# Optimization experiments

Measured on AMD Instinct MI355X. Metric: run time of the kernel, lower is better.

The kernel has to match this reference:

```python
import jax, jax.numpy as jnp
import numpy as np
from jax import lax

NUM_ANCHORS = 3
NUM_CLASSES = 80
SCORE_THRESH = 0.3
NMS_THRESH = 0.45
TOPK = 128  # max kept candidates per class per image (fixed-shape NMS)
REDUCTIONS = (8, 16, 32)
_ANCHORS = np.array([[12, 16], [19, 36], [40, 28], [36, 75], [76, 55], [72, 146],
                     [142, 110], [192, 243], [459, 401]], dtype=np.float32).reshape(3, 3, 2)


def _decode(pred, anchors):
    # pred: [b, A*(5+C), h, w]; anchors: [A,2] already divided by reduction
    b, c, h, w = pred.shape
    p = pred.reshape(b, NUM_ANCHORS, 5 + NUM_CLASSES, h * w).transpose(0, 1, 3, 2)  # [b,A,hw,5+C]
    gx = (jnp.arange(h * w) % w).astype(p.dtype)   # grid x offset per flattened cell
    gy = (jnp.arange(h * w) // w).astype(p.dtype)  # grid y offset
    cx = (jax.nn.sigmoid(p[..., 0]) + gx) / w
    cy = (jax.nn.sigmoid(p[..., 1]) + gy) / h
    bw = jnp.exp(p[..., 2]) * (anchors[:, 0] / w)[None, :, None]
    bh = jnp.exp(p[..., 3]) * (anchors[:, 1] / h)[None, :, None]
    x1 = cx - 0.5 * bw
    y1 = cy - 0.5 * bh
    boxes = jnp.stack([x1, y1, x1 + bw, y1 + bh], axis=-1)  # [b,A,hw,4] xyxy, normalized
    scores = jax.nn.sigmoid(p[..., 4])[..., None] * jax.nn.sigmoid(p[..., 5:])  # [b,A,hw,C]
    return boxes, scores


def _nms_single(boxes, probs):
    # boxes: [N,4]; probs: [N] with below-threshold entries masked to -1.
    # Greedy NMS on top-K candidates sorted by score (same math as the numpy loop).
    vals, idx = lax.top_k(probs, TOPK)
    bx = boxes[idx]                                            # [K,4] sorted by score desc
    area = (bx[:, 2] - bx[:, 0]) * (bx[:, 3] - bx[:, 1])
    tl = jnp.maximum(bx[:, None, :2], bx[None, :, :2])
    br = jnp.minimum(bx[:, None, 2:], bx[None, :, 2:])
    whi = jnp.clip(br - tl, 0.0)
    inter = whi[..., 0] * whi[..., 1]
    iou = inter / (area[:, None] + area[None, :] - inter)      # [K,K]
    ar = jnp.arange(TOPK)

    def step(p, i):
        sup = (iou[i] > NMS_THRESH) & (ar > i) & (p[i] > 0)
        return jnp.where(sup, -1.0, p), None

    p, _ = lax.scan(step, vals, ar)
    keep = p > 0
    return jnp.where(keep[:, None], bx, 0.0), jnp.where(keep, p, 0.0)


def reference(preds0, preds1, preds2):
    boxes_list, score_list = [], []
    for pred, red, anc in zip((preds0, preds1, preds2), REDUCTIONS, _ANCHORS):
        bx, sc = _decode(pred, jnp.asarray(anc) / red)
        boxes_list.append(bx)
        score_list.append(sc)
    boxes = jnp.concatenate(boxes_list, axis=2)
    scores = jnp.concatenate(score_list, axis=2)
    b = boxes.shape[0]
    boxes = boxes.reshape(b, -1, 4)              # [b, N, 4],  N = A * sum(hw)
    scores = scores.reshape(b, -1, NUM_CLASSES)  # [b, N, C]
    probs = jnp.where(scores > SCORE_THRESH, scores, -1.0)
    per_class = jax.vmap(_nms_single, in_axes=(None, 1))        # map over classes
    out_boxes, out_scores = jax.vmap(per_class)(boxes, probs)   # [b,C,K,4], [b,C,K]
    cls_id = jnp.broadcast_to(
        jnp.arange(NUM_CLASSES, dtype=out_boxes.dtype)[None, :, None], out_scores.shape)
    # [b, C, K, 6] = (x1, y1, x2, y2, score, class_id); zeroed rows = no detection
    return jnp.concatenate([out_boxes, out_scores[..., None], cls_id[..., None]], axis=-1)


def setup_inputs():
    key = jax.random.key(0)
    k0, k1, k2 = jax.random.split(key, 3)
    C = NUM_ANCHORS * (5 + NUM_CLASSES)
    return {
        "preds0": jax.random.normal(k0, (16, C, 76, 76), jnp.float32),
        "preds1": jax.random.normal(k1, (16, C, 38, 38), jnp.float32),
        "preds2": jax.random.normal(k2, (16, C, 19, 19), jnp.float32),
    }
```

## Files before the change

kernel.cpp:

```cpp
#include <hip/hip_runtime.h>
#include <math.h>
#include <stdint.h>

#define BATCH 16
#define NCLS 80
#define SUMHW 7581
#define NN 22743
#define ASTRIDE 7584
#define PADNN (3 * ASTRIDE)
#define TOPK 128
#define CAP 1024
#define WCAP 320
#define GMAX (4 * WCAP)
#define PRUNECAP 512
#define KEYBASE 0x3E800000u
#define KB2     0x3F180000u
#define SBITS   0x3F19999Au

typedef float f32x4 __attribute__((ext_vector_type(4)));

__device__ __forceinline__ float sigf(float x) {
    float e = (float)exp(-(double)x);
    return 1.0f / (1.0f + e);
}
__device__ __forceinline__ float expf_cr(float x) {
    return (float)exp((double)x);
}

struct DecParams { float aw[9]; float ah[9]; };

__global__ __launch_bounds__(256) void decode_kernel(
        const float* __restrict__ p0, const float* __restrict__ p1,
        const float* __restrict__ p2,
        float* __restrict__ so_arr, float* __restrict__ xthr_arr) {
    int blk = blockIdx.x;
    int b = blk / 27;
    int rem = blk % 27;
    int a = rem / 9;
    int seg = rem % 9;
    int s, segi;
    if (seg < 6)      { s = 0; segi = seg; }
    else if (seg < 8) { s = 1; segi = seg - 6; }
    else              { s = 2; segi = 0; }
    const int HW_[3]  = {5776, 1444, 361};
    const int OFF_[3] = {0, 5776, 7220};
    const float* __restrict__ pr = (s == 0) ? p0 : (s == 1) ? p1 : p2;
    int HW = HW_[s], OFF = OFF_[s];
    int t = threadIdx.x;

    auto mkthr = [](float so) {
        float thr = __int_as_float(0x7F800000);
        if (so > 0.59999f) {
            double arg = (double)so / 0.59999 - 1.0;
            thr = __double2float_rd(-log(arg));
        }
        return thr;
    };

    if (s != 2) {
        int cell0 = segi * 1024 + t * 4;
        if (cell0 >= HW) return;
        const float4* ob4 =
            (const float4*)(pr + ((size_t)b * 255 + (size_t)a * 85 + 4) * (size_t)HW);
        float4 ov = ob4[cell0 >> 2];
        float4 sov, thv;
        sov.x = sigf(ov.x); thv.x = mkthr(sov.x);
        sov.y = sigf(ov.y); thv.y = mkthr(sov.y);
        sov.z = sigf(ov.z); thv.z = mkthr(sov.z);
        sov.w = sigf(ov.w); thv.w = mkthr(sov.w);
        size_t pidx = (size_t)b * PADNN + a * ASTRIDE + OFF + cell0;
        *(float4*)(so_arr + pidx)   = sov;
        *(float4*)(xthr_arr + pidx) = thv;
    } else {
        const float* ob = pr + ((size_t)b * 255 + (size_t)a * 85 + 4) * 361;
        for (int i = t; i < 361; i += 256) {
            float so = sigf(ob[i]);
            size_t pidx = (size_t)b * PADNN + a * ASTRIDE + 7220 + i;
            so_arr[pidx] = so;
            xthr_arr[pidx] = mkthr(so);
        }
    }
}

__global__ __launch_bounds__(256) void select_nms_kernel(
        const float* __restrict__ p0, const float* __restrict__ p1,
        const float* __restrict__ p2,
        const float* __restrict__ so_arr,
        const float* __restrict__ xthr_arr,
        DecParams dp,
        float* __restrict__ out) {
    __shared__ __attribute__((aligned(16))) unsigned long long wn64[4 * WCAP];
    unsigned long long* skeyF = wn64;
    __shared__ unsigned int kbuf[GMAX];
    __shared__ unsigned long long skeyM[PRUNECAP];
    __shared__ unsigned long long sorted[TOPK];
    __shared__ unsigned long long mskp[2 * TOPK];
    __shared__ float4 bxs4[TOPK];
    __shared__ float pvs[TOPK];
    __shared__ unsigned int hist[512];
    __shared__ unsigned int wtot[4];
    __shared__ unsigned int wvc[4];
    __shared__ unsigned long long aliveLDS[2];
    __shared__ unsigned int sh_bin, sh_above, gcount;

    int t = threadIdx.x;
    int w = t >> 6, lane = t & 63;
    int bid = blockIdx.x;
    int b = bid / NCLS;
    int c = bid % NCLS;

    if (t < 4) wvc[t] = 0;
    for (int i = t; i < 512; i += 256) hist[i] = 0;
    __syncthreads();

    auto wavePush = [&](unsigned m, f32x4 A0, f32x4 A1, f32x4 A2, int cellb) {
        unsigned cnt = (unsigned)__popc(m);
        unsigned inc = cnt;
#pragma unroll
        for (int d = 1; d < 64; d <<= 1) {
            unsigned o = (unsigned)__shfl_up((int)inc, d);
            if (lane >= d) inc += o;
        }
        unsigned wt = (unsigned)__shfl((int)inc, 63);
        if (wt) {
            unsigned base = 0;
            if (lane == 63) base = atomicAdd(&wvc[w], wt);
            base = (unsigned)__shfl((int)base, 63);
            unsigned pos = base + inc - cnt;
            unsigned long long* wl = wn64 + w * WCAP;
#define PKW(bit, val, nn) \
            if (m & (bit)) { if (pos < WCAP) wl[pos] = \
                (((unsigned long long)__float_as_uint(val)) << 32) | (unsigned)(nn); \
                pos++; }
            PKW(0x001u, A0.x, cellb + 0)
            PKW(0x002u, A0.y, cellb + 1)
            PKW(0x004u, A0.z, cellb + 2)
            PKW(0x008u, A0.w, cellb + 3)
            PKW(0x010u, A1.x, SUMHW + cellb + 0)
            PKW(0x020u, A1.y, SUMHW + cellb + 1)
            PKW(0x040u, A1.z, SUMHW + cellb + 2)
            PKW(0x080u, A1.w, SUMHW + cellb + 3)
            PKW(0x100u, A2.x, 2 * SUMHW + cellb + 0)
            PKW(0x200u, A2.y, 2 * SUMHW + cellb + 1)
            PKW(0x400u, A2.z, 2 * SUMHW + cellb + 2)
            PKW(0x800u, A2.w, 2 * SUMHW + cellb + 3)
#undef PKW
        }
    };
    auto cmpMask = [&](f32x4 A0, f32x4 A1, f32x4 A2,
                       f32x4 Q0, f32x4 Q1, f32x4 Q2) -> unsigned {
        unsigned m = 0;
        m |= (A0.x > Q0.x) ? 0x001u : 0u;  m |= (A0.y > Q0.y) ? 0x002u : 0u;
        m |= (A0.z > Q0.z) ? 0x004u : 0u;  m |= (A0.w > Q0.w) ? 0x008u : 0u;
        m |= (A1.x > Q1.x) ? 0x010u : 0u;  m |= (A1.y > Q1.y) ? 0x020u : 0u;
        m |= (A1.z > Q1.z) ? 0x040u : 0u;  m |= (A1.w > Q1.w) ? 0x080u : 0u;
        m |= (A2.x > Q2.x) ? 0x100u : 0u;  m |= (A2.y > Q2.y) ? 0x200u : 0u;
        m |= (A2.z > Q2.z) ? 0x400u : 0u;  m |= (A2.w > Q2.w) ? 0x800u : 0u;
        return m;
    };

    auto scanBlock = [&](const float* __restrict__ pr, int HW, int OFF) {
        const int nq = HW >> 2;
        unsigned long long bx0 = (unsigned long long)(uintptr_t)
            (pr + ((size_t)b * 255 + 0 * 85 + 5 + (size_t)c) * (size_t)HW);
        unsigned long long bx1 = (unsigned long long)(uintptr_t)
            (pr + ((size_t)b * 255 + 1 * 85 + 5 + (size_t)c) * (size_t)HW);
        unsigned long long bx2 = (unsigned long long)(uintptr_t)
            (pr + ((size_t)b * 255 + 2 * 85 + 5 + (size_t)c) * (size_t)HW);
        unsigned long long bq0 = (unsigned long long)(uintptr_t)
            (xthr_arr + (size_t)b * PADNN + 0 * ASTRIDE + OFF);
        unsigned long long bq1 = (unsigned long long)(uintptr_t)
            (xthr_arr + (size_t)b * PADNN + 1 * ASTRIDE + OFF);
        unsigned long long bq2 = (unsigned long long)(uintptr_t)
            (xthr_arr + (size_t)b * PADNN + 2 * ASTRIDE + OFF);
        const int nIter = (nq + 511) >> 9;
        for (int k2 = 0; k2 < nIter; ++k2) {
            int i1 = t + (k2 << 9);
            int i2 = i1 + 256;
            bool a1 = i1 < nq, a2 = i2 < nq;
            unsigned vo1 = (unsigned)(a1 ? i1 : (nq - 1)) << 4;
            unsigned vo2 = (unsigned)(a2 ? i2 : (nq - 1)) << 4;
            f32x4 x0, x1, x2, x3, x4, x5, q0, q1, q2, q3, q4, q5;
            asm volatile(
                "global_load_dwordx4 %0, %12, %14\n\t"
                "global_load_dwordx4 %1, %12, %15\n\t"
                "global_load_dwordx4 %2, %12, %16\n\t"
                "global_load_dwordx4 %3, %13, %14\n\t"
                "global_load_dwordx4 %4, %13, %15\n\t"
                "global_load_dwordx4 %5, %13, %16\n\t"
                "global_load_dwordx4 %6, %12, %17\n\t"
                "global_load_dwordx4 %7, %12, %18\n\t"
                "global_load_dwordx4 %8, %12, %19\n\t"
                "global_load_dwordx4 %9, %13, %17\n\t"
                "global_load_dwordx4 %10, %13, %18\n\t"
                "global_load_dwordx4 %11, %13, %19\n\t"
                "s_waitcnt vmcnt(0)"
                : "=&v"(x0), "=&v"(x1), "=&v"(x2), "=&v"(x3), "=&v"(x4), "=&v"(x5),
                  "=&v"(q0), "=&v"(q1), "=&v"(q2), "=&v"(q3), "=&v"(q4), "=&v"(q5)
                : "v"(vo1), "v"(vo2), "s"(bx0), "s"(bx1), "s"(bx2),
                  "s"(bq0), "s"(bq1), "s"(bq2));
            unsigned m1 = cmpMask(x0, x1, x2, q0, q1, q2); if (!a1) m1 = 0;
            unsigned m2 = cmpMask(x3, x4, x5, q3, q4, q5); if (!a2) m2 = 0;
            wavePush(m1, x0, x1, x2, OFF + 4 * i1);
            wavePush(m2, x3, x4, x5, OFF + 4 * i2);
        }
    };
    scanBlock(p0, 5776, 0);
    scanBlock(p1, 1444, 5776);
#pragma unroll
    for (int a = 0; a < 3; ++a) {
        const float* __restrict__ cp =
            p2 + ((size_t)b * 255 + (size_t)a * 85 + 5 + (size_t)c) * 361;
        const float* __restrict__ xt = xthr_arr + (size_t)b * PADNN + a * ASTRIDE + 7220;
        int n0 = a * SUMHW + 7220;
        for (int i = t; i < 361; i += 256) {
            float xv = cp[i];
            if (xv > xt[i]) {
                unsigned pos = atomicAdd(&wvc[w], 1u);
                if (pos < WCAP) wn64[w * WCAP + pos] =
                    (((unsigned long long)__float_as_uint(xv)) << 32) | (unsigned)(n0 + i);
            }
        }
    }
    __syncthreads();

    unsigned cw0 = wvc[0], cw1 = wvc[1], cw2 = wvc[2], cw3 = wvc[3];
    bool ovf = (cw0 > WCAP) || (cw1 > WCAP) || (cw2 > WCAP) || (cw3 > WCAP);
    unsigned G = cw0 + cw1 + cw2 + cw3;
    bool fb = ovf || (G < TOPK);

    auto suffixScan = [&](unsigned mt, unsigned& total) -> unsigned {
        __syncthreads();
        unsigned sfx = mt;
#pragma unroll
        for (int d = 1; d < 64; d <<= 1) {
            unsigned o = (unsigned)__shfl_down((int)sfx, d);
            if (lane + d < 64) sfx += o;
        }
        if (lane == 0) wtot[w] = sfx;
        __syncthreads();
        unsigned cross = 0;
#pragma unroll
        for (int ww = 0; ww < 4; ++ww) if (ww > w) cross += wtot[ww];
        total = wtot[0] + wtot[1] + wtot[2] + wtot[3];
        return sfx + cross;
    };

    auto rankSelect2 = [&](const unsigned long long* sk, unsigned Gc) {
        if (t < TOPK) sorted[t] = 0ULL;
        __syncthreads();
        if ((unsigned)t < Gc) {
            unsigned long long o0 = sk[t];
            bool v1 = (unsigned)(t + 256) < Gc;
            unsigned long long o1 = v1 ? sk[t + 256] : 0ULL;
            unsigned r0 = 0, r1 = 0;
            for (unsigned j = 0; j < Gc; ++j) {
                unsigned long long kj = sk[j];
                r0 += (kj > o0); r1 += (kj > o1);
            }
            if (r0 < TOPK) sorted[r0] = o0;
            if (v1 && r1 < TOPK) sorted[r1] = o1;
        }
        __syncthreads();
    };
    auto rankSelect4 = [&](const unsigned long long* sk, unsigned Gc) {
        if (t < TOPK) sorted[t] = 0ULL;
        __syncthreads();
        if ((unsigned)t < Gc) {
            unsigned i1 = t + 256, i2 = t + 512, i3 = t + 768;
            bool v1 = i1 < Gc, v2 = i2 < Gc, v3 = i3 < Gc;
            unsigned long long o0 = sk[t];
            unsigned long long o1 = v1 ? sk[i1] : 0ULL;
            unsigned long long o2 = v2 ? sk[i2] : 0ULL;
            unsigned long long o3 = v3 ? sk[i3] : 0ULL;
            unsigned r0 = 0, r1 = 0, r2 = 0, r3 = 0;
            for (unsigned j = 0; j < Gc; ++j) {
                unsigned long long kj = sk[j];
                r0 += (kj > o0); r1 += (kj > o1); r2 += (kj > o2); r3 += (kj > o3);
            }
            if (r0 < TOPK) sorted[r0] = o0;
            if (v1 && r1 < TOPK) sorted[r1] = o1;
            if (v2 && r2 < TOPK) sorted[r2] = o2;
            if (v3 && r3 < TOPK) sorted[r3] = o3;
        }
        __syncthreads();
    };

    if (!fb) {
        unsigned woff = 0;
        if (w > 0) woff += cw0;
        if (w > 1) woff += cw1;
        if (w > 2) woff += cw2;
        unsigned mycnt = (w == 0) ? cw0 : (w == 1) ? cw1 : (w == 2) ? cw2 : cw3;
        for (unsigned i = lane; i < mycnt; i += 64) {
            unsigned long long e = wn64[w * WCAP + i];
            float x = __uint_as_float((unsigned)(e >> 32));
            unsigned n = (unsigned)(e & 0xFFFFFFFFu);
            unsigned a = n / SUMHW;
            unsigned r = n - a * SUMHW;
            float so = so_arr[(size_t)b * PADNN + a * ASTRIDE + r];
            float st = 1.0f / (1.0f + __expf(-x));
            unsigned key = __float_as_uint(st * so);
            kbuf[woff + i] = key;
            unsigned bin = (key - KB2) >> 14;
            if (bin > 511u) bin = 511u;
            atomicAdd(&hist[bin], 1u);
        }
        if (t == 0) gcount = 0;
        __syncthreads();

        unsigned m0 = hist[2 * t], m1 = hist[2 * t + 1];
        unsigned total;
        unsigned si = suffixScan(m0 + m1, total);
        unsigned se = si - (m0 + m1);
        if (se < TOPK && TOPK <= si) {
            if (TOPK <= se + m1) { sh_bin = 2 * t + 1; sh_above = se; }
            else                 { sh_bin = 2 * t;     sh_above = se + m1; }
        }
        __syncthreads();
        unsigned B1 = sh_bin, above1 = sh_above;
        unsigned cntB = hist[B1];
        unsigned binlo = KB2 + (B1 << 14);
        if (above1 + cntB > PRUNECAP - 64) {
            fb = true;
        } else {
            unsigned gth = binlo - 256;
            unsigned b1e = cw0, b2e = cw0 + cw1, b3e = b2e + cw2;
            for (unsigned i = t; i < G; i += 256) {
                if (kbuf[i] >= gth) {
                    unsigned pos = atomicAdd(&gcount, 1u);
                    if (pos < PRUNECAP) {
                        unsigned w2, off2;
                        if (i < b1e)      { w2 = 0; off2 = i; }
                        else if (i < b2e) { w2 = 1; off2 = i - b1e; }
                        else if (i < b3e) { w2 = 2; off2 = i - b2e; }
                        else              { w2 = 3; off2 = i - b3e; }
                        unsigned long long e = wn64[w2 * WCAP + off2];
                        float x = __uint_as_float((unsigned)(e >> 32));
                        unsigned n = (unsigned)(e & 0xFFFFFFFFu);
                        unsigned a = n / SUMHW;
                        unsigned r = n - a * SUMHW;
                        float so = so_arr[(size_t)b * PADNN + a * ASTRIDE + r];
                        float ex = so * sigf(x);
                        skeyM[pos] = (ex > 0.3f)
                            ? (((unsigned long long)__float_as_uint(ex) << 32) |
                               (unsigned)(~n))
                            : (unsigned long long)(unsigned)(~n);
                    }
                }
            }
            __syncthreads();
            if (gcount > PRUNECAP) fb = true;
            if (!fb) {
                unsigned Gc = gcount;
                rankSelect2(skeyM, Gc);
                bool ok = (Gc >= TOPK) && ((unsigned)(sorted[TOPK - 1] >> 32) >= SBITS);
                if (!ok) fb = true;
            }
        }
    }

    if (fb) {
        auto scanScalar = [&](auto&& body) {
#pragma unroll
            for (int s = 0; s < 3; ++s) {
                const float* __restrict__ pr = (s == 0) ? p0 : (s == 1) ? p1 : p2;
                const int HW  = (s == 0) ? 5776 : (s == 1) ? 1444 : 361;
                const int OFF = (s == 0) ? 0 : (s == 1) ? 5776 : 7220;
#pragma unroll
                for (int a = 0; a < 3; ++a) {
                    const float* __restrict__ cp =
                        pr + ((size_t)b * 255 + (size_t)a * 85 + 5 + (size_t)c) * (size_t)HW;
                    const float* __restrict__ sop =
                        so_arr + (size_t)b * PADNN + a * ASTRIDE + OFF;
                    int n0 = a * SUMHW + OFF;
                    for (int i = t; i < HW; i += 256) {
                        float so = sop[i];
                        if (so <= 0.2999f) continue;
                        float x = cp[i];
                        float st = 1.0f / (1.0f + __expf(-x));
                        float sca = st * so;
                        if (sca > 0.2999f) body(sca, x, so, n0 + i);
                    }
                }
            }
        };
        __syncthreads();
        for (int i = t; i < 512; i += 256) hist[i] = 0;
        if (t == 0) gcount = 0;
        __syncthreads();
        scanScalar([&](float sca, float, float, int) {
            unsigned bin = (__float_as_uint(sca) - KEYBASE) >> 15;
            if (bin > 511u) bin = 511u;
            atomicAdd(&hist[bin], 1u);
        });
        __syncthreads();
        unsigned m0 = hist[2 * t], m1 = hist[2 * t + 1];
        unsigned total;
        unsigned si = suffixScan(m0 + m1, total);
        bool gatherAll = (total < TOPK);
        unsigned gth = 0;
        if (!gatherAll) {
            unsigned se = si - (m0 + m1);
            if (se < TOPK && TOPK <= si) {
                if (TOPK <= se + m1) { sh_bin = 2 * t + 1; sh_above = se; }
                else                 { sh_bin = 2 * t;     sh_above = se + m1; }
            }
            __syncthreads();
            unsigned B1 = sh_bin, above1 = sh_above;
            unsigned cntB = hist[B1];
            unsigned binlo = KEYBASE + (B1 << 15);
            __syncthreads();
            if (above1 + cntB <= 768) {
                gth = binlo - 256;
            } else {
                if (t < 256) hist[t] = 0;
                __syncthreads();
                scanScalar([&](float sca, float, float, int) {
                    unsigned key = __float_as_uint(sca);
                    if (((key - KEYBASE) >> 15) == B1) {
                        unsigned sub = (key - binlo) >> 7;
                        if (sub > 255u) sub = 255u;
                        atomicAdd(&hist[sub], 1u);
                    }
                });
                __syncthreads();
                unsigned R2 = TOPK - above1;
                unsigned sl = hist[t];
                unsigned tot2;
                unsigned si2 = suffixScan(sl, tot2);
                unsigned se2 = si2 - sl;
                if (se2 < R2 && R2 <= si2) sh_bin = (unsigned)t;
                __syncthreads();
                gth = binlo + (sh_bin << 7) - 256;
            }
        }
        __syncthreads();
        scanScalar([&](float sca, float x, float so, int n) {
            unsigned key = __float_as_uint(sca);
            if (gatherAll || key >= gth) {
                unsigned pos = atomicAdd(&gcount, 1u);
                if (pos < CAP) {
                    float ex = so * sigf(x);
                    skeyF[pos] = (ex > 0.3f)
                        ? (((unsigned long long)__float_as_uint(ex) << 32) |
                           (unsigned)(~(unsigned)n))
                        : (unsigned long long)(unsigned)(~(unsigned)n);
                }
            }
        });
        __syncthreads();
        unsigned Gc = gcount < CAP ? gcount : CAP;
        rankSelect4(skeyF, Gc);
    }

    if (t < TOPK) {
        unsigned long long e = sorted[t];
        bool vld = (e != 0ULL);
        float sc = __uint_as_float((unsigned)(e >> 32));
        unsigned n = ~(unsigned)(e & 0xFFFFFFFFu);
        float4 bb = make_float4(0.f, 0.f, 0.f, 0.f);
        if (vld) {
            unsigned a = n / SUMHW;
            unsigned r = n - a * SUMHW;
            int s, S, HW, off; const float* pr;
            if (r < 5776u)      { s = 0; S = 76; HW = 5776; off = 0;    pr = p0; }
            else if (r < 7220u) { s = 1; S = 38; HW = 1444; off = 5776; pr = p1; }
            else                { s = 2; S = 19; HW = 361;  off = 7220; pr = p2; }
            int cell = (int)r - off;
            const float* pb = pr + ((size_t)b * 255 + (size_t)a * 85) * (size_t)HW + cell;
            float tx = pb[0];
            float ty = pb[(size_t)HW];
            float tw = pb[(size_t)2 * HW];
            float th = pb[(size_t)3 * HW];
            float Sf = (float)S;
            float gx = (float)(cell % S);
            float gy = (float)(cell / S);
            float cx = (sigf(tx) + gx) / Sf;
            float cy = (sigf(ty) + gy) / Sf;
            float aw = dp.aw[s * 3 + a], ah = dp.ah[s * 3 + a];
            float bw = expf_cr(tw) * aw;
            float bh = expf_cr(th) * ah;
            float x1 = cx - 0.5f * bw;
            float y1 = cy - 0.5f * bh;
            bb = make_float4(x1, y1, x1 + bw, y1 + bh);
        }
        bxs4[t] = bb;
        pvs[t] = vld ? sc : -1.0f;
    }
    __syncthreads();

    {
        int i = t >> 1, h = t & 1;
        unsigned long long m = 0;
        if (!(h == 0 && i >= 64)) {
            float4 bi = bxs4[i];
            float ai = (bi.z - bi.x) * (bi.w - bi.y);
            int jb = h << 6;
            int kstart = (h == 0) ? (i + 1) : ((i >= 64) ? (i - 63) : 0);
            for (int k = kstart; k < 64; ++k) {
                int j = jb + k;
                float4 bj = bxs4[j];
                float aj = (bj.z - bj.x) * (bj.w - bj.y);
                float xx1 = fmaxf(bi.x, bj.x), yy1 = fmaxf(bi.y, bj.y);
                float xx2 = fminf(bi.z, bj.z), yy2 = fminf(bi.w, bj.w);
                float ww = fmaxf(xx2 - xx1, 0.0f), hh = fmaxf(yy2 - yy1, 0.0f);
                float inter = ww * hh;
                float iou = inter / (ai + aj - inter);
                if (j > i && iou > 0.45f) m |= (1ull << k);
            }
        }
        mskp[(i << 1) | h] = m;
    }
    __syncthreads();
    if (t < 64) {
        unsigned long long A0 = __ballot(pvs[t] > 0.0f);
        unsigned long long A1 = __ballot(pvs[t + 64] > 0.0f);
        for (int i = 0; i < 64; ++i) {
            if ((A0 >> i) & 1) { A0 &= ~mskp[i << 1]; A1 &= ~mskp[(i << 1) | 1]; }
        }
        for (int i = 0; i < 64; ++i) {
            if ((A1 >> i) & 1) { A1 &= ~mskp[((64 + i) << 1) | 1]; }
        }
        if (t == 0) { aliveLDS[0] = A0; aliveLDS[1] = A1; }
    }
    __syncthreads();

    unsigned long long A0 = aliveLDS[0], A1 = aliveLDS[1];
    float* o = out + (size_t)bid * TOPK * 6;
    for (int i = t; i < TOPK; i += 256) {
        bool alive = (i < 64) ? ((A0 >> i) & 1) : ((A1 >> (i - 64)) & 1);
        float p = pvs[i];
        bool kept = alive && (p > 0.0f);
        float4 bb = bxs4[i];
        o[i * 6 + 0] = kept ? bb.x : 0.0f;
        o[i * 6 + 1] = kept ? bb.y : 0.0f;
        o[i * 6 + 2] = kept ? bb.z : 0.0f;
        o[i * 6 + 3] = kept ? bb.w : 0.0f;
        o[i * 6 + 4] = kept ? p : 0.0f;
        o[i * 6 + 5] = (float)c;
    }
}

extern "C" void kernel_launch(void* const* d_in, const int* in_sizes, int n_in,
                              void* d_out, int out_size, void* d_ws, size_t ws_size,
                              hipStream_t stream) {
    const float* p0 = (const float*)d_in[0];
    const float* p1 = (const float*)d_in[1];
    const float* p2 = (const float*)d_in[2];
    float* out = (float*)d_out;

    char* ws = (char*)d_ws;
    float* so_arr = (float*)ws;
    float* xthr   = (float*)(ws + 1456128ull);

    static const float ANC[3][3][2] = {
        {{12, 16}, {19, 36}, {40, 28}},
        {{36, 75}, {76, 55}, {72, 146}},
        {{142, 110}, {192, 243}, {459, 401}},
    };
    static const int RED[3] = {8, 16, 32};
    static const int SS[3]  = {76, 38, 19};

    DecParams dp;
    for (int s = 0; s < 3; ++s)
        for (int a = 0; a < 3; ++a) {
            float Sf = (float)SS[s];
            dp.aw[s * 3 + a] = (ANC[s][a][0] / (float)RED[s]) / Sf;
            dp.ah[s * 3 + a] = (ANC[s][a][1] / (float)RED[s]) / Sf;
        }

    decode_kernel<<<BATCH * 27, 256, 0, stream>>>(p0, p1, p2, so_arr, xthr);
    select_nms_kernel<<<BATCH * NCLS, 256, 0, stream>>>(p0, p1, p2, so_arr, xthr, dp, out);
}
```

Measured before the change: 68.15 us.

## Split candidate scan into separate 4-way parallel kernel feeding tail NMS via global list

The fused per-(batch,class) select+NMS kernel is split in two. A scan kernel launches four blocks per (batch,class), each scanning a quarter of the cells. Each block stages threshold-passing candidates in LDS and appends them to a per-class global list through an atomic counter. A tail kernel then reads that list for the histogram, top-K selection and NMS. This is meant to raise parallelism and occupancy for the bandwidth-bound scan, at the cost of a memset, an extra launch, global atomics, and a round trip of candidates through global memory.

New measurement: 89.20 us. 30.9% more time.

```diff
diff --git a/kernel.cpp b/kernel.cpp
--- a/kernel.cpp
+++ b/kernel.cpp
@@ -10,8 +10,8 @@
 #define PADNN (3 * ASTRIDE)
 #define TOPK 128
 #define CAP 1024
-#define WCAP 320
-#define GMAX (4 * WCAP)
+#define WSCAP 128
+#define GCAP 2048
 #define PRUNECAP 512
 #define KEYBASE 0x3E800000u
 #define KB2     0x3F180000u
@@ -82,56 +82,47 @@
     }
 }
 
-__global__ __launch_bounds__(256) void select_nms_kernel(
+__global__ __launch_bounds__(256) void scan_kernel(
         const float* __restrict__ p0, const float* __restrict__ p1,
         const float* __restrict__ p2,
-        const float* __restrict__ so_arr,
         const float* __restrict__ xthr_arr,
-        DecParams dp,
-        float* __restrict__ out) {
-    __shared__ __attribute__((aligned(16))) unsigned long long wn64[4 * WCAP];
-    unsigned long long* skeyF = wn64;
-    __shared__ unsigned int kbuf[GMAX];
-    __shared__ unsigned long long skeyM[PRUNECAP];
-    __shared__ unsigned long long sorted[TOPK];
-    __shared__ unsigned long long mskp[2 * TOPK];
-    __shared__ float4 bxs4[TOPK];
-    __shared__ float pvs[TOPK];
-    __shared__ unsigned int hist[512];
-    __shared__ unsigned int wtot[4];
+        unsigned long long* __restrict__ glist, unsigned int* __restrict__ gcnt) {
+    __shared__ unsigned long long stg[4][WSCAP];
     __shared__ unsigned int wvc[4];
-    __shared__ unsigned long long aliveLDS[2];
-    __shared__ unsigned int sh_bin, sh_above, gcount;
-
-    int t = threadIdx.x;
-    int w = t >> 6, lane = t & 63;
-    int bid = blockIdx.x;
-    int b = bid / NCLS;
-    int c = bid % NCLS;
+
+    int blk = blockIdx.x;
+    int bc = blk >> 2;
+    int chunk = blk & 3;
+    int b = bc / NCLS;
+    int c = bc % NCLS;
+    int t = threadIdx.x, w = t >> 6, lane = t & 63;
 
     if (t < 4) wvc[t] = 0;
-    for (int i = t; i < 512; i += 256) hist[i] = 0;
     __syncthreads();
 
-    auto wavePush = [&](unsigned m, f32x4 A0, f32x4 A1, f32x4 A2, int cellb) {
-        unsigned cnt = (unsigned)__popc(m);
-        unsigned inc = cnt;
-#pragma unroll
-        for (int d = 1; d < 64; d <<= 1) {
-            unsigned o = (unsigned)__shfl_up((int)inc, d);
-            if (lane >= d) inc += o;
-        }
-        unsigned wt = (unsigned)__shfl((int)inc, 63);
-        if (wt) {
-            unsigned base = 0;
-            if (lane == 63) base = atomicAdd(&wvc[w], wt);
-            base = (unsigned)__shfl((int)base, 63);
-            unsigned pos = base + inc - cnt;
-            unsigned long long* wl = wn64 + w * WCAP;
-#define PKW(bit, val, nn) \
-            if (m & (bit)) { if (pos < WCAP) wl[pos] = \
-                (((unsigned long long)__float_as_uint(val)) << 32) | (unsigned)(nn); \
-                pos++; }
+    auto pushItem = [&](float xv, unsigned nn, unsigned pos) {
+        unsigned long long e =
+            ((unsigned long long)__float_as_uint(xv) << 32) | nn;
+        if (pos < WSCAP) stg[w][pos] = e;
+        else {
+            unsigned gp = atomicAdd(&gcnt[bc], 1u);
+            if (gp < GCAP) glist[(size_t)bc * GCAP + gp] = e;
+        }
+    };
+    auto cmpPushB = [&](f32x4 A0, f32x4 A1, f32x4 A2,
+                        f32x4 Q0, f32x4 Q1, f32x4 Q2, int cellb, bool act) {
+        unsigned m = 0;
+        if (act) {
+            m |= (A0.x > Q0.x) ? 0x001u : 0u;  m |= (A0.y > Q0.y) ? 0x002u : 0u;
+            m |= (A0.z > Q0.z) ? 0x004u : 0u;  m |= (A0.w > Q0.w) ? 0x008u : 0u;
+            m |= (A1.x > Q1.x) ? 0x010u : 0u;  m |= (A1.y > Q1.y) ? 0x020u : 0u;
+            m |= (A1.z > Q1.z) ? 0x040u : 0u;  m |= (A1.w > Q1.w) ? 0x080u : 0u;
+            m |= (A2.x > Q2.x) ? 0x100u : 0u;  m |= (A2.y > Q2.y) ? 0x200u : 0u;
+            m |= (A2.z > Q2.z) ? 0x400u : 0u;  m |= (A2.w > Q2.w) ? 0x800u : 0u;
+        }
+        if (m) {
+            unsigned pos = atomicAdd(&wvc[w], (unsigned)__popc(m));
+#define PKW(bit, val, nn) if (m & (bit)) { pushItem(val, (unsigned)(nn), pos); pos++; }
             PKW(0x001u, A0.x, cellb + 0)
             PKW(0x002u, A0.y, cellb + 1)
             PKW(0x004u, A0.z, cellb + 2)
@@ -147,20 +138,11 @@
 #undef PKW
         }
     };
-    auto cmpMask = [&](f32x4 A0, f32x4 A1, f32x4 A2,
-                       f32x4 Q0, f32x4 Q1, f32x4 Q2) -> unsigned {
-        unsigned m = 0;
-        m |= (A0.x > Q0.x) ? 0x001u : 0u;  m |= (A0.y > Q0.y) ? 0x002u : 0u;
-        m |= (A0.z > Q0.z) ? 0x004u : 0u;  m |= (A0.w > Q0.w) ? 0x008u : 0u;
-        m |= (A1.x > Q1.x) ? 0x010u : 0u;  m |= (A1.y > Q1.y) ? 0x020u : 0u;
-        m |= (A1.z > Q1.z) ? 0x040u : 0u;  m |= (A1.w > Q1.w) ? 0x080u : 0u;
-        m |= (A2.x > Q2.x) ? 0x100u : 0u;  m |= (A2.y > Q2.y) ? 0x200u : 0u;
-        m |= (A2.z > Q2.z) ? 0x400u : 0u;  m |= (A2.w > Q2.w) ? 0x800u : 0u;
-        return m;
-    };
-
-    auto scanBlock = [&](const float* __restrict__ pr, int HW, int OFF) {
+
+    auto scanStrip = [&](const float* __restrict__ pr, int HW, int OFF) {
         const int nq = HW >> 2;
+        const int qlo = (nq * chunk) >> 2;
+        const int qhi = (nq * (chunk + 1)) >> 2;
         unsigned long long bx0 = (unsigned long long)(uintptr_t)
             (pr + ((size_t)b * 255 + 0 * 85 + 5 + (size_t)c) * (size_t)HW);
         unsigned long long bx1 = (unsigned long long)(uintptr_t)
@@ -173,61 +155,93 @@
             (xthr_arr + (size_t)b * PADNN + 1 * ASTRIDE + OFF);
         unsigned long long bq2 = (unsigned long long)(uintptr_t)
             (xthr_arr + (size_t)b * PADNN + 2 * ASTRIDE + OFF);
-        const int nIter = (nq + 511) >> 9;
-        for (int k2 = 0; k2 < nIter; ++k2) {
-            int i1 = t + (k2 << 9);
-            int i2 = i1 + 256;
-            bool a1 = i1 < nq, a2 = i2 < nq;
-            unsigned vo1 = (unsigned)(a1 ? i1 : (nq - 1)) << 4;
-            unsigned vo2 = (unsigned)(a2 ? i2 : (nq - 1)) << 4;
-            f32x4 x0, x1, x2, x3, x4, x5, q0, q1, q2, q3, q4, q5;
+        const int nIter = (qhi - qlo + 255) >> 8;
+        for (int k = 0; k < nIter; ++k) {
+            int i = qlo + t + (k << 8);
+            bool act = i < qhi;
+            unsigned vo = (unsigned)(act ? i : (qhi - 1)) << 4;
+            f32x4 x0, x1, x2, q0, q1, q2;
             asm volatile(
-                "global_load_dwordx4 %0, %12, %14\n\t"
-                "global_load_dwordx4 %1, %12, %15\n\t"
-                "global_load_dwordx4 %2, %12, %16\n\t"
-                "global_load_dwordx4 %3, %13, %14\n\t"
-                "global_load_dwordx4 %4, %13, %15\n\t"
-                "global_load_dwordx4 %5, %13, %16\n\t"
-                "global_load_dwordx4 %6, %12, %17\n\t"
-                "global_load_dwordx4 %7, %12, %18\n\t"
-                "global_load_dwordx4 %8, %12, %19\n\t"
-                "global_load_dwordx4 %9, %13, %17\n\t"
-                "global_load_dwordx4 %10, %13, %18\n\t"
-                "global_load_dwordx4 %11, %13, %19\n\t"
+                "global_load_dwordx4 %0, %6, %7\n\t"
+                "global_load_dwordx4 %1, %6, %8\n\t"
+                "global_load_dwordx4 %2, %6, %9\n\t"
+                "global_load_dwordx4 %3, %6, %10\n\t"
+                "global_load_dwordx4 %4, %6, %11\n\t"
+                "global_load_dwordx4 %5, %6, %12\n\t"
                 "s_waitcnt vmcnt(0)"
-                : "=&v"(x0), "=&v"(x1), "=&v"(x2), "=&v"(x3), "=&v"(x4), "=&v"(x5),
-                  "=&v"(q0), "=&v"(q1), "=&v"(q2), "=&v"(q3), "=&v"(q4), "=&v"(q5)
-                : "v"(vo1), "v"(vo2), "s"(bx0), "s"(bx1), "s"(bx2),
+                : "=&v"(x0), "=&v"(x1), "=&v"(x2),
+                  "=&v"(q0), "=&v"(q1), "=&v"(q2)
+                : "v"(vo), "s"(bx0), "s"(bx1), "s"(bx2),
                   "s"(bq0), "s"(bq1), "s"(bq2));
-            unsigned m1 = cmpMask(x0, x1, x2, q0, q1, q2); if (!a1) m1 = 0;
-            unsigned m2 = cmpMask(x3, x4, x5, q3, q4, q5); if (!a2) m2 = 0;
-            wavePush(m1, x0, x1, x2, OFF + 4 * i1);
-            wavePush(m2, x3, x4, x5, OFF + 4 * i2);
-        }
-    };
-    scanBlock(p0, 5776, 0);
-    scanBlock(p1, 1444, 5776);
+            cmpPushB(x0, x1, x2, q0, q1, q2, OFF + 4 * i, act);
+        }
+    };
+    scanStrip(p0, 5776, 0);
+    scanStrip(p1, 1444, 5776);
+    {
+        const int clo = (361 * chunk) >> 2;
+        const int chi = (361 * (chunk + 1)) >> 2;
 #pragma unroll
-    for (int a = 0; a < 3; ++a) {
-        const float* __restrict__ cp =
-            p2 + ((size_t)b * 255 + (size_t)a * 85 + 5 + (size_t)c) * 361;
-        const float* __restrict__ xt = xthr_arr + (size_t)b * PADNN + a * ASTRIDE + 7220;
-        int n0 = a * SUMHW + 7220;
-        for (int i = t; i < 361; i += 256) {
-            float xv = cp[i];
-            if (xv > xt[i]) {
-                unsigned pos = atomicAdd(&wvc[w], 1u);
-                if (pos < WCAP) wn64[w * WCAP + pos] =
-                    (((unsigned long long)__float_as_uint(xv)) << 32) | (unsigned)(n0 + i);
+        for (int a = 0; a < 3; ++a) {
+            const float* __restrict__ cp =
+                p2 + ((size_t)b * 255 + (size_t)a * 85 + 5 + (size_t)c) * 361;
+            const float* __restrict__ xt =
+                xthr_arr + (size_t)b * PADNN + a * ASTRIDE + 7220;
+            for (int i = clo + t; i < chi; i += 256) {
+                float xv = cp[i];
+                if (xv > xt[i]) {
+                    unsigned pos = atomicAdd(&wvc[w], 1u);
+                    pushItem(xv, (unsigned)(a * SUMHW + 7220 + i), pos);
+                }
             }
         }
     }
     __syncthreads();
 
-    unsigned cw0 = wvc[0], cw1 = wvc[1], cw2 = wvc[2], cw3 = wvc[3];
-    bool ovf = (cw0 > WCAP) || (cw1 > WCAP) || (cw2 > WCAP) || (cw3 > WCAP);
-    unsigned G = cw0 + cw1 + cw2 + cw3;
-    bool fb = ovf || (G < TOPK);
+    unsigned mycnt = wvc[w]; if (mycnt > WSCAP) mycnt = WSCAP;
+    unsigned base = 0;
+    if (lane == 0) base = atomicAdd(&gcnt[bc], mycnt);
+    base = (unsigned)__shfl((int)base, 0);
+    for (unsigned i = lane; i < mycnt; i += 64) {
+        unsigned p = base + i;
+        if (p < GCAP) glist[(size_t)bc * GCAP + p] = stg[w][i];
+    }
+}
+
+__global__ __launch_bounds__(256) void tail_kernel(
+        const float* __restrict__ p0, const float* __restrict__ p1,
+        const float* __restrict__ p2,
+        const float* __restrict__ so_arr,
+        const unsigned long long* __restrict__ glist,
+        const unsigned int* __restrict__ gcnt,
+        DecParams dp,
+        float* __restrict__ out) {
+    __shared__ unsigned int kbuf[GCAP];
+    unsigned long long* skeyF = (unsigned long long*)kbuf;
+    __shared__ unsigned long long skeyM[PRUNECAP];
+    __shared__ unsigned long long sorted[TOPK];
+    __shared__ unsigned long long mskp[2 * TOPK];
+    __shared__ float4 bxs4[TOPK];
+    __shared__ float pvs[TOPK];
+    __shared__ unsigned int hist[512];
+    __shared__ unsigned int wtot[4];
+    __shared__ unsigned long long aliveLDS[2];
+    __shared__ unsigned int sh_bin, sh_above, gcount;
+
+    int t = threadIdx.x;
+    int w = t >> 6, lane = t & 63;
+    int bid = blockIdx.x;
+    int b = bid / NCLS;
+    int c = bid % NCLS;
+
+    for (int i = t; i < 512; i += 256) hist[i] = 0;
+    if (t == 0) gcount = 0;
+    __syncthreads();
+
+    unsigned gcv = gcnt[bid];
+    unsigned G = gcv < GCAP ? gcv : GCAP;
+    bool fb = (gcv > GCAP) || (G < TOPK);
+    const unsigned long long* gl = glist + (size_t)bid * GCAP;
 
     auto suffixScan = [&](unsigned mt, unsigned& total) -> unsigned {
         __syncthreads();
@@ -287,13 +301,8 @@
     };
 
     if (!fb) {
-        unsigned woff = 0;
-        if (w > 0) woff += cw0;
-        if (w > 1) woff += cw1;
-        if (w > 2) woff += cw2;
-        unsigned mycnt = (w == 0) ? cw0 : (w == 1) ? cw1 : (w == 2) ? cw2 : cw3;
-        for (unsigned i = lane; i < mycnt; i += 64) {
-            unsigned long long e = wn64[w * WCAP + i];
+        for (unsigned i = t; i < G; i += 256) {
+            unsigned long long e = gl[i];
             float x = __uint_as_float((unsigned)(e >> 32));
             unsigned n = (unsigned)(e & 0xFFFFFFFFu);
             unsigned a = n / SUMHW;
@@ -301,12 +310,11 @@
             float so = so_arr[(size_t)b * PADNN + a * ASTRIDE + r];
             float st = 1.0f / (1.0f + __expf(-x));
             unsigned key = __float_as_uint(st * so);
-            kbuf[woff + i] = key;
+            kbuf[i] = key;
             unsigned bin = (key - KB2) >> 14;
             if (bin > 511u) bin = 511u;
             atomicAdd(&hist[bin], 1u);
         }
-        if (t == 0) gcount = 0;
         __syncthreads();
 
         unsigned m0 = hist[2 * t], m1 = hist[2 * t + 1];
@@ -325,17 +333,11 @@
             fb = true;
         } else {
             unsigned gth = binlo - 256;
-            unsigned b1e = cw0, b2e = cw0 + cw1, b3e = b2e + cw2;
             for (unsigned i = t; i < G; i += 256) {
                 if (kbuf[i] >= gth) {
                     unsigned pos = atomicAdd(&gcount, 1u);
                     if (pos < PRUNECAP) {
-                        unsigned w2, off2;
-                        if (i < b1e)      { w2 = 0; off2 = i; }
-                        else if (i < b2e) { w2 = 1; off2 = i - b1e; }
-                        else if (i < b3e) { w2 = 2; off2 = i - b2e; }
-                        else              { w2 = 3; off2 = i - b3e; }
-                        unsigned long long e = wn64[w2 * WCAP + off2];
+                        unsigned long long e = gl[i];
                         float x = __uint_as_float((unsigned)(e >> 32));
                         unsigned n = (unsigned)(e & 0xFFFFFFFFu);
                         unsigned a = n / SUMHW;
@@ -553,6 +555,8 @@
     char* ws = (char*)d_ws;
     float* so_arr = (float*)ws;
     float* xthr   = (float*)(ws + 1456128ull);
+    unsigned int* gcnt = (unsigned int*)(ws + 2912256ull);
+    unsigned long long* glist = (unsigned long long*)(ws + 2920448ull);
 
     static const float ANC[3][3][2] = {
         {{12, 16}, {19, 36}, {40, 28}},
@@ -570,6 +574,9 @@
             dp.ah[s * 3 + a] = (ANC[s][a][1] / (float)RED[s]) / Sf;
         }
 
+    hipMemsetAsync(gcnt, 0, BATCH * NCLS * sizeof(unsigned int), stream);
     decode_kernel<<<BATCH * 27, 256, 0, stream>>>(p0, p1, p2, so_arr, xthr);
-    select_nms_kernel<<<BATCH * NCLS, 256, 0, stream>>>(p0, p1, p2, so_arr, xthr, dp, out);
+    scan_kernel<<<BATCH * NCLS * 4, 256, 0, stream>>>(p0, p1, p2, xthr, glist, gcnt);
+    tail_kernel<<<BATCH * NCLS, 256, 0, stream>>>(p0, p1, p2, so_arr,
+                                                  glist, gcnt, dp, out);
 }
```
